# Optimization experiments

Measured on AMD Instinct MI355X. Metric: run time of the kernel, lower is better.

The kernel has to match this reference:

```python
import jax, jax.numpy as jnp
import numpy as np

DIM = 512
HEADS = 8
DIM_HEAD = 64
INNER = HEADS * DIM_HEAD  # 512
TOPK_FRAC = 0.7
SCALE = DIM_HEAD ** -0.5


def setup_inputs() -> dict:
    key = jax.random.key(0)
    k1, k2, k3, k4 = jax.random.split(key, 4)
    B, N = 4, 1024
    x = jax.random.normal(k1, (B, N, DIM), dtype=jnp.float32)
    # nn.Linear(dim, inner*3, bias=False): weight [3*inner, dim]; store transposed for x @ W
    w_qkv = jax.random.normal(k2, (DIM, 3 * INNER), dtype=jnp.float32) * (DIM ** -0.5)
    # to_out Linear(inner, dim) with bias
    w_out = jax.random.normal(k3, (INNER, DIM), dtype=jnp.float32) * (INNER ** -0.5)
    b_out = jax.random.normal(k4, (DIM,), dtype=jnp.float32) * 0.01
    return {"x": x, "w_qkv": w_qkv, "w_out": w_out, "b_out": b_out}


def reference(x, w_qkv, w_out, b_out):
    B, N, _ = x.shape
    H, D = HEADS, DIM_HEAD
    qkv = x @ w_qkv  # [B, N, 3*INNER]
    q, k, v = jnp.split(qkv, 3, axis=-1)
    # 'b n (h d) -> b h n d'
    reshape = lambda t: t.reshape(B, N, H, D).transpose(0, 2, 1, 3)
    q, k, v = reshape(q), reshape(k), reshape(v)
    dots = jnp.einsum('bhid,bhjd->bhij', q, k) * SCALE  # [B, H, N, N]
    # per-row top-k masking (kNN attention)
    kk = int(N * TOPK_FRAC)
    _, idx = jax.lax.top_k(dots, kk)  # [B, H, N, kk]
    bi = jnp.arange(B)[:, None, None, None]
    hi = jnp.arange(H)[None, :, None, None]
    ii = jnp.arange(N)[None, None, :, None]
    mask = jnp.zeros_like(dots).at[bi, hi, ii, idx].set(1.0)
    dots = jnp.where(mask > 0, dots, jnp.float32(-jnp.inf))
    attn = jax.nn.softmax(dots, axis=-1)
    out = jnp.einsum('bhij,bhjd->bhid', attn, v)  # [B, H, N, D]
    out = out.transpose(0, 2, 1, 3).reshape(B, N, H * D)  # 'b h n d -> b n (h d)'
    return out @ w_out + b_out
```

## Files before the change

kernel.cpp:

```cpp
#include <hip/hip_runtime.h>
#include <cstddef>

#define B_      4
#define N_      1024
#define DIM_    512
#define H_      8
#define D_      64
#define INNER_  512
#define TRIPLE_ 1536
#define KK_     716
#define SCALE_  0.125f

typedef short bf16x8 __attribute__((ext_vector_type(8)));
typedef float f32x4  __attribute__((ext_vector_type(4)));
typedef unsigned short ushort_t;
typedef ushort_t us8 __attribute__((ext_vector_type(8)));

__device__ __forceinline__ unsigned short bf16_rne(float f) {
    unsigned u = __float_as_uint(f);
    return (unsigned short)((u + 0x7FFFu + ((u >> 16) & 1u)) >> 16);
}
__device__ __forceinline__ float bf16_f(unsigned short s) {
    return __uint_as_float((unsigned)s << 16);
}
__device__ __forceinline__ unsigned f2key(float f) {
    unsigned u = __float_as_uint(f);
    return u ^ ((u & 0x80000000u) ? 0xFFFFFFFFu : 0x80000000u);
}
__device__ __forceinline__ float key2f(unsigned k) {
    unsigned u = (k & 0x80000000u) ? (k ^ 0x80000000u) : ~k;
    return __uint_as_float(u);
}
__device__ __forceinline__ int wave_count(int lc) {
    int c = __popcll(__ballot(lc & 1));
    c += __popcll(__ballot(lc & 2)) << 1;
    c += __popcll(__ballot(lc & 4)) << 2;
    c += __popcll(__ballot(lc & 8)) << 3;
    c += __popcll(__ballot(lc & 16)) << 4;
    return c;
}
__device__ __forceinline__ int count_ge(const unsigned* key, unsigned kt) {
    int lc = 0;
#pragma unroll
    for (int m = 0; m < 16; ++m) lc += (key[m] >= kt) ? 1 : 0;
    return wave_count(lc);
}
__device__ __forceinline__ unsigned bisect_exact(const unsigned* key,
                                                 bool hlo, bool hhi,
                                                 float tlo, float thi) {
    unsigned klo = hlo ? f2key(tlo) : 0u;
    unsigned khi = hhi ? f2key(thi) : 0xFFFFFFFFu;
    while (khi - klo > 1u) {
        const unsigned km = klo + ((khi - klo) >> 1);
        const int c = count_ge(key, km);
        if (c >= KK_) { klo = km; if (c == KK_) break; }
        else khi = km;
    }
    return klo;
}
__device__ __forceinline__ void topk2(const unsigned* key0, const unsigned* key1,
                                      float mu0, float sg0, float mu1, float sg1,
                                      unsigned& out0, unsigned& out1) {
    bool done0 = false, done1 = false;
    float tlo0 = 0.f, thi0 = 0.f, tlo1 = 0.f, thi1 = 0.f;
    int   clo0 = 0,   chi0 = 0,   clo1 = 0,   chi1 = 0;
    bool  hlo0 = false, hhi0 = false, hlo1 = false, hhi1 = false;
    float t0 = mu0 - 0.52189f * sg0;
    float t1 = mu1 - 0.52189f * sg1;
    unsigned res0 = 0u, res1 = 0u;
    for (int it = 0; it < 10; ++it) {
        if (done0 & done1) break;
        const unsigned kt0 = f2key(t0);
        const unsigned kt1 = f2key(t1);
        int lc0 = 0, lc1 = 0;
#pragma unroll
        for (int m = 0; m < 16; ++m) {
            lc0 += (key0[m] >= kt0) ? 1 : 0;
            lc1 += (key1[m] >= kt1) ? 1 : 0;
        }
        const int c0 = wave_count(lc0);
        const int c1 = wave_count(lc1);
        if (!done0) {
            if (c0 == KK_) { res0 = kt0; done0 = true; }
            else {
                if (c0 > KK_) { tlo0 = t0; clo0 = c0; hlo0 = true; }
                else          { thi0 = t0; chi0 = c0; hhi0 = true; }
                float tn;
                if (hlo0 && hhi0) {
                    tn = tlo0 + (thi0 - tlo0) * ((float)(clo0 - KK_) / (float)(clo0 - chi0));
                } else {
                    const float z    = (t0 - mu0) / sg0;
                    const float dens = fmaxf(408.5f * __expf(-0.5f * z * z) / sg0, 1.f);
                    tn = t0 + (float)(c0 - KK_) / dens;
                }
                if (hlo0 && !(tn > tlo0)) tn = hhi0 ? 0.5f * (tlo0 + thi0) : tlo0 + 0.25f * sg0;
                if (hhi0 && !(tn < thi0)) tn = hlo0 ? 0.5f * (tlo0 + thi0) : thi0 - 0.25f * sg0;
                t0 = tn;
            }
        }
        if (!done1) {
            if (c1 == KK_) { res1 = kt1; done1 = true; }
            else {
                if (c1 > KK_) { tlo1 = t1; clo1 = c1; hlo1 = true; }
                else          { thi1 = t1; chi1 = c1; hhi1 = true; }
                float tn;
                if (hlo1 && hhi1) {
                    tn = tlo1 + (thi1 - tlo1) * ((float)(clo1 - KK_) / (float)(clo1 - chi1));
                } else {
                    const float z    = (t1 - mu1) / sg1;
                    const float dens = fmaxf(408.5f * __expf(-0.5f * z * z) / sg1, 1.f);
                    tn = t1 + (float)(c1 - KK_) / dens;
                }
                if (hlo1 && !(tn > tlo1)) tn = hhi1 ? 0.5f * (tlo1 + thi1) : tlo1 + 0.25f * sg1;
                if (hhi1 && !(tn < thi1)) tn = hlo1 ? 0.5f * (tlo1 + thi1) : thi1 - 0.25f * sg1;
                t1 = tn;
            }
        }
    }
    if (!done0) res0 = bisect_exact(key0, hlo0, hhi0, tlo0, thi0);
    if (!done1) res1 = bisect_exact(key1, hlo1, hhi1, tlo1, thi1);
    out0 = res0;
    out1 = res1;
}
__device__ __forceinline__ void split8(const float* __restrict__ src,
                                       bf16x8& h8, bf16x8& l8) {
    float4 a = *(const float4*)src;
    float4 b = *(const float4*)(src + 4);
    float v[8] = {a.x, a.y, a.z, a.w, b.x, b.y, b.z, b.w};
#pragma unroll
    for (int i = 0; i < 8; ++i) {
        ushort_t hb = bf16_rne(v[i]);
        h8[i] = (short)hb;
        l8[i] = (short)bf16_rne(v[i] - bf16_f(hb));
    }
}

__global__ __launch_bounds__(256) void prep_split(const float* __restrict__ Wq,
                                                  const float* __restrict__ Wo,
                                                  ushort_t* __restrict__ WqTh,
                                                  ushort_t* __restrict__ WqTl,
                                                  ushort_t* __restrict__ WoTh,
                                                  ushort_t* __restrict__ WoTl) {
    __shared__ float tile[32][33];
    const int wb = blockIdx.x;
    const int bx = wb & 63, by = wb >> 6;
    const bool isQ = bx < 48;
    const int  nb  = (isQ ? bx : bx - 48) * 32;
    const int  kb  = by * 32;
    const int  Nn  = isQ ? TRIPLE_ : DIM_;
    const float* W = isQ ? Wq : Wo;
    ushort_t* Th   = isQ ? WqTh : WoTh;
    ushort_t* Tl   = isQ ? WqTl : WoTl;
    const int tx = threadIdx.x & 31, ty = threadIdx.x >> 5;
    for (int yy = ty; yy < 32; yy += 8)
        tile[yy][tx] = W[(size_t)(kb + yy) * Nn + nb + tx];
    __syncthreads();
    for (int yy = ty; yy < 32; yy += 8) {
        float v = tile[tx][yy];
        ushort_t hb = bf16_rne(v);
        size_t idx = (size_t)(nb + yy) * DIM_ + kb + tx;
        Th[idx] = hb;
        Tl[idx] = bf16_rne(v - bf16_f(hb));
    }
}

__global__ __launch_bounds__(256) void gemm_qkv_mfma(
    const float* __restrict__ X,
    const ushort_t* __restrict__ Wh, const ushort_t* __restrict__ Wl,
    ushort_t* __restrict__ Qh, ushort_t* __restrict__ Ql,
    ushort_t* __restrict__ Kh, ushort_t* __restrict__ Kl,
    ushort_t* __restrict__ Vt) {
    __shared__ ushort_t stile[4][4608];
    __shared__ ushort_t BshH[2][2048];
    __shared__ ushort_t BshL[2][2048];
    const int t = threadIdx.x, w = t >> 6, l = t & 63;
    const int ln = l & 15, quad = l >> 4;
    const int n0 = blockIdx.y * 64;
    const int m0 = blockIdx.x * 128 + w * 32;
    f32x4 acc[2][4] = {};
    {
        const size_t xrow0 = (size_t)(m0 + ln) * DIM_;
        const size_t xrow1 = (size_t)(m0 + 16 + ln) * DIM_;
        const int srow = t >> 2;
        const int sk   = (t & 3) << 3;
        const size_t gb = (size_t)(n0 + srow) * DIM_ + sk;
        us8 nh = *(const us8*)&Wh[gb];
        us8 nl = *(const us8*)&Wl[gb];
        *(us8*)&BshH[0][t * 8] = nh;
        *(us8*)&BshL[0][t * 8] = nl;
        int cur = 0;
        for (int k0 = 0; k0 < DIM_; k0 += 32) {
            const bool more = (k0 + 32) < DIM_;
            const size_t gnext = gb + (size_t)(more ? k0 + 32 : 0);
            nh = *(const us8*)&Wh[gnext];
            nl = *(const us8*)&Wl[gnext];
            __syncthreads();
            const int ko = k0 + quad * 8;
            bf16x8 ah0, al0, ah1, al1;
            split8(&X[xrow0 + ko], ah0, al0);
            split8(&X[xrow1 + ko], ah1, al1);
#pragma unroll
            for (int j = 0; j < 4; ++j) {
                const int slot = (((j << 4) + ln) << 5) + (quad << 3);
                bf16x8 bh = *(const bf16x8*)&BshH[cur][slot];
                bf16x8 bl = *(const bf16x8*)&BshL[cur][slot];
                acc[0][j] = __builtin_amdgcn_mfma_f32_16x16x32_bf16(ah0, bh, acc[0][j], 0, 0, 0);
                acc[0][j] = __builtin_amdgcn_mfma_f32_16x16x32_bf16(al0, bh, acc[0][j], 0, 0, 0);
                acc[0][j] = __builtin_amdgcn_mfma_f32_16x16x32_bf16(ah0, bl, acc[0][j], 0, 0, 0);
                acc[1][j] = __builtin_amdgcn_mfma_f32_16x16x32_bf16(ah1, bh, acc[1][j], 0, 0, 0);
                acc[1][j] = __builtin_amdgcn_mfma_f32_16x16x32_bf16(al1, bh, acc[1][j], 0, 0, 0);
                acc[1][j] = __builtin_amdgcn_mfma_f32_16x16x32_bf16(ah1, bl, acc[1][j], 0, 0, 0);
            }
            if (more) {
                *(us8*)&BshH[cur ^ 1][t * 8] = nh;
                *(us8*)&BshL[cur ^ 1][t * 8] = nl;
            }
            cur ^= 1;
        }
    }
    const int sec = n0 >> 9;
    const int h   = (n0 >> 6) & 7;
    ushort_t* tw  = stile[w];
    const int b = m0 >> 10, nnb = m0 & 1023;
    if (sec < 2) {
        ushort_t* Hp = sec ? Kh : Qh;
        ushort_t* Lp = sec ? Kl : Ql;
        const float qsc = sec ? 1.0f : SCALE_;
#pragma unroll
        for (int i = 0; i < 2; ++i)
#pragma unroll
            for (int j = 0; j < 4; ++j)
#pragma unroll
                for (int g = 0; g < 4; ++g) {
                    const float v = acc[i][j][g] * qsc;
                    const ushort_t hb = bf16_rne(v);
                    const ushort_t lb = bf16_rne(v - bf16_f(hb));
                    const int tok = i * 16 + quad * 4 + g;
                    const int d   = j * 16 + ln;
                    tw[tok * 72 + d]        = hb;
                    tw[2304 + tok * 72 + d] = lb;
                }
        __syncthreads();
        const size_t rowbase = ((size_t)(b * 8 + h) * 1024 + nnb) * 64;
        const int dd = (l & 7) * 8;
#pragma unroll
        for (int s = 0; s < 4; ++s) {
            const int tl = s * 8 + (l >> 3);
            const size_t off = rowbase + (size_t)tl * 64 + dd;
            *(us8*)&Hp[off] = *(const us8*)&tw[tl * 72 + dd];
            *(us8*)&Lp[off] = *(const us8*)&tw[2304 + tl * 72 + dd];
        }
    } else {
#pragma unroll
        for (int i = 0; i < 2; ++i)
#pragma unroll
            for (int j = 0; j < 4; ++j)
#pragma unroll
                for (int g = 0; g < 4; ++g)
                    tw[(j * 16 + ln) * 40 + i * 16 + quad * 4 + g] = bf16_rne(acc[i][j][g]);
        __syncthreads();
        const size_t vbase = (size_t)(b * 8 + h) * 65536 + nnb;
#pragma unroll
        for (int p = 0; p < 2; ++p) {
            const int d = (p << 5) + (l >> 1);
            const int c = (l & 1) << 4;
            ushort_t* dst = &Vt[vbase + (size_t)d * 1024 + c];
            *(us8*)dst       = *(const us8*)&tw[d * 40 + c];
            *(us8*)(dst + 8) = *(const us8*)&tw[d * 40 + c + 8];
        }
    }
}

__global__ __launch_bounds__(256) void gemm_out_mfma(
    const ushort_t* __restrict__ Ah, const ushort_t* __restrict__ Al,
    const ushort_t* __restrict__ Wh, const ushort_t* __restrict__ Wl,
    const float* __restrict__ bias, float* __restrict__ C) {
    __shared__ ushort_t BshH[2][2048];
    __shared__ ushort_t BshL[2][2048];
    const int t = threadIdx.x, w = t >> 6, l = t & 63;
    const int ln = l & 15, quad = l >> 4;
    const int n0 = blockIdx.y * 64;
    const int m0 = blockIdx.x * 64 + w * 16;
    f32x4 acc[4] = {};
    {
        const size_t arow0 = (size_t)(m0 + ln) * INNER_;
        const int srow = t >> 2;
        const int sk   = (t & 3) << 3;
        const size_t gb = (size_t)(n0 + srow) * INNER_ + sk;
        us8 nh = *(const us8*)&Wh[gb];
        us8 nl = *(const us8*)&Wl[gb];
        *(us8*)&BshH[0][t * 8] = nh;
        *(us8*)&BshL[0][t * 8] = nl;
        int cur = 0;
        for (int k0 = 0; k0 < INNER_; k0 += 32) {
            const bool more = (k0 + 32) < INNER_;
            const size_t gnext = gb + (size_t)(more ? k0 + 32 : 0);
            nh = *(const us8*)&Wh[gnext];
            nl = *(const us8*)&Wl[gnext];
            __syncthreads();
            const int ko = k0 + quad * 8;
            bf16x8 ah0 = *(const bf16x8*)&Ah[arow0 + ko];
            bf16x8 al0 = *(const bf16x8*)&Al[arow0 + ko];
#pragma unroll
            for (int j = 0; j < 4; ++j) {
                const int slot = (((j << 4) + ln) << 5) + (quad << 3);
                bf16x8 bh = *(const bf16x8*)&BshH[cur][slot];
                bf16x8 bl = *(const bf16x8*)&BshL[cur][slot];
                acc[j] = __builtin_amdgcn_mfma_f32_16x16x32_bf16(ah0, bh, acc[j], 0, 0, 0);
                acc[j] = __builtin_amdgcn_mfma_f32_16x16x32_bf16(al0, bh, acc[j], 0, 0, 0);
                acc[j] = __builtin_amdgcn_mfma_f32_16x16x32_bf16(ah0, bl, acc[j], 0, 0, 0);
            }
            if (more) {
                *(us8*)&BshH[cur ^ 1][t * 8] = nh;
                *(us8*)&BshL[cur ^ 1][t * 8] = nl;
            }
            cur ^= 1;
        }
    }
#pragma unroll
    for (int j = 0; j < 4; ++j) {
        const int col = n0 + j * 16 + ln;
        const float bb = bias[col];
#pragma unroll
        for (int g = 0; g < 4; ++g) {
            const int token = m0 + quad * 4 + g;
            C[(size_t)token * DIM_ + col] = acc[j][g] + bb;
        }
    }
}

__global__ __launch_bounds__(512)
__attribute__((amdgpu_waves_per_eu(4, 4)))
void attn_mfma(const ushort_t* __restrict__ Qh,
               const ushort_t* __restrict__ Ql,
               const ushort_t* __restrict__ Kh,
               const ushort_t* __restrict__ Kl,
               const ushort_t* __restrict__ Vt,
               ushort_t* __restrict__ Oh,
               ushort_t* __restrict__ Ol) {
    __shared__ float sdots[16 * 1024];
    __shared__ float spartial[4][16][17];

    const int t    = threadIdx.x;
    const int w    = t >> 6;
    const int l    = t & 63;
    const int ln   = l & 15;
    const int quad = l >> 4;
    const int wg   = blockIdx.x;
    const int bh   = wg & 31;
    const int i0   = (wg >> 5) << 4;

    const size_t bhoff = (size_t)bh << 16;

    const ushort_t* qp  = Qh + bhoff + (size_t)(i0 + ln) * 64 + (quad << 3);
    const ushort_t* qlp = Ql + bhoff + (size_t)(i0 + ln) * 64 + (quad << 3);
    bf16x8 qh0 = *(const bf16x8*)qp;
    bf16x8 qh1 = *(const bf16x8*)(qp + 32);
    bf16x8 ql0 = *(const bf16x8*)qlp;
    bf16x8 ql1 = *(const bf16x8*)(qlp + 32);

    const int dblk  = w & 3;
    const int jbase = (w & 4) << 7;
    const ushort_t* vp =
        Vt + bhoff + (size_t)((dblk << 4) + ln) * 1024 + (quad << 3) + jbase;
    bf16x8 vpre[8];

    for (int tt = 0; tt < 8; ++tt) {
        const int j0 = ((w << 3) + tt) << 4;
        const ushort_t* kp  = Kh + bhoff + (size_t)(j0 + ln) * 64 + (quad << 3);
        const ushort_t* klp = Kl + bhoff + (size_t)(j0 + ln) * 64 + (quad << 3);
        bf16x8 kh0 = *(const bf16x8*)kp;
        bf16x8 kh1 = *(const bf16x8*)(kp + 32);
        bf16x8 kl0 = *(const bf16x8*)klp;
        bf16x8 kl1 = *(const bf16x8*)(klp + 32);
        f32x4 acc = {0.f, 0.f, 0.f, 0.f};
        acc = __builtin_amdgcn_mfma_f32_16x16x32_bf16(qh0, kh0, acc, 0, 0, 0);
        acc = __builtin_amdgcn_mfma_f32_16x16x32_bf16(qh1, kh1, acc, 0, 0, 0);
        acc = __builtin_amdgcn_mfma_f32_16x16x32_bf16(qh0, kl0, acc, 0, 0, 0);
        acc = __builtin_amdgcn_mfma_f32_16x16x32_bf16(qh1, kl1, acc, 0, 0, 0);
        acc = __builtin_amdgcn_mfma_f32_16x16x32_bf16(ql0, kh0, acc, 0, 0, 0);
        acc = __builtin_amdgcn_mfma_f32_16x16x32_bf16(ql1, kh1, acc, 0, 0, 0);
#pragma unroll
        for (int g = 0; g < 4; ++g) {
            const int row = (quad << 2) + g;
            sdots[(row << 10) + ((j0 + ln) ^ ((row & 7) << 2))] = acc[g];
        }
    }
    __syncthreads();

    ushort_t* sP = (ushort_t*)sdots;
    {
        const int r0 = w << 1, r1 = r0 | 1;
        const int swz0 = (r0 & 7) << 2, swz1 = (r1 & 7) << 2;
        const float* s0 = &sdots[r0 << 10];
        const float* s1 = &sdots[r1 << 10];
        unsigned key0[16], key1[16];
        float sa0 = 0.f, sb0 = 0.f, sa1 = 0.f, sb1 = 0.f;
#pragma unroll
        for (int m = 0; m < 4; ++m) {
            f32x4 kv0 = *(const f32x4*)&s0[((l << 2) + (m << 8)) ^ swz0];
            f32x4 kv1 = *(const f32x4*)&s1[((l << 2) + (m << 8)) ^ swz1];
#pragma unroll
            for (int i = 0; i < 4; ++i) {
                key0[(m << 2) + i] = f2key(kv0[i]);
                key1[(m << 2) + i] = f2key(kv1[i]);
                sa0 += kv0[i];
                sb0 += kv0[i] * kv0[i];
                sa1 += kv1[i];
                sb1 += kv1[i] * kv1[i];
            }
        }
#pragma unroll
        for (int off = 32; off; off >>= 1) {
            sa0 += __shfl_xor(sa0, off, 64);
            sb0 += __shfl_xor(sb0, off, 64);
            sa1 += __shfl_xor(sa1, off, 64);
            sb1 += __shfl_xor(sb1, off, 64);
        }
        const float mu0 = sa0 * (1.0f / 1024.f);
        const float sg0 = sqrtf(fmaxf(sb0 * (1.0f / 1024.f) - mu0 * mu0, 1e-20f));
        const float mu1 = sa1 * (1.0f / 1024.f);
        const float sg1 = sqrtf(fmaxf(sb1 * (1.0f / 1024.f) - mu1 * mu1, 1e-20f));

        unsigned res0, res1;
        topk2(key0, key1, mu0, sg0, mu1, sg1, res0, res1);

        const float thr0 = key2f(res0), thr1 = key2f(res1);
        float pv0[16], pv1[16];
        float ls0 = 0.f, ls1 = 0.f;
#pragma unroll
        for (int m = 0; m < 16; ++m) {
            float p0 = (key0[m] >= res0) ? __expf(key2f(key0[m]) - thr0) : 0.f;
            float p1 = (key1[m] >= res1) ? __expf(key2f(key1[m]) - thr1) : 0.f;
            pv0[m] = p0;
            pv1[m] = p1;
            ls0 += p0;
            ls1 += p1;
        }
#pragma unroll
        for (int p = 0; p < 8; ++p)
            vpre[p] = *(const bf16x8*)(vp + p * 32);
#pragma unroll
        for (int off = 32; off; off >>= 1) {
            ls0 += __shfl_xor(ls0, off, 64);
            ls1 += __shfl_xor(ls1, off, 64);
        }
        const float inv0 = 1.f / ls0, inv1 = 1.f / ls1;
#pragma unroll
        for (int m = 0; m < 4; ++m) {
            const int g0 = ((l >> 1) + (m << 5)) ^ (r0 & 7);
            const int g1 = ((l >> 1) + (m << 5)) ^ (r1 & 7);
            ushort4 pk0 = make_ushort4(bf16_rne(pv0[(m << 2) + 0] * inv0),
                                       bf16_rne(pv0[(m << 2) + 1] * inv0),
                                       bf16_rne(pv0[(m << 2) + 2] * inv0),
                                       bf16_rne(pv0[(m << 2) + 3] * inv0));
            ushort4 pk1 = make_ushort4(bf16_rne(pv1[(m << 2) + 0] * inv1),
                                       bf16_rne(pv1[(m << 2) + 1] * inv1),
                                       bf16_rne(pv1[(m << 2) + 2] * inv1),
                                       bf16_rne(pv1[(m << 2) + 3] * inv1));
            *(ushort4*)&sP[(r0 << 11) + (g0 << 3) + ((l & 1) << 2)] = pk0;
            *(ushort4*)&sP[(r1 << 11) + (g1 << 3) + ((l & 1) << 2)] = pk1;
        }
    }
    __syncthreads();

    const int prow = ln << 11;
    const int rsw  = ln & 7;
    bf16x8 vnx[8];
#pragma unroll
    for (int p = 0; p < 8; ++p)
        vnx[p] = *(const bf16x8*)(vp + 256 + p * 32);
    f32x4 oa[4] = {};
    __builtin_amdgcn_s_setprio(1);
#pragma unroll
    for (int p = 0; p < 8; ++p) {
        const int j0 = p * 32;
        const int g = ((jbase + j0) >> 3) + quad;
        bf16x8 af = *(const bf16x8*)&sP[prow + ((g ^ rsw) << 3)];
        oa[p & 3] = __builtin_amdgcn_mfma_f32_16x16x32_bf16(af, vpre[p], oa[p & 3], 0, 0, 0);
    }
#pragma unroll
    for (int p = 0; p < 8; ++p) {
        const int j0 = 256 + p * 32;
        const int g = ((jbase + j0) >> 3) + quad;
        bf16x8 af = *(const bf16x8*)&sP[prow + ((g ^ rsw) << 3)];
        oa[p & 3] = __builtin_amdgcn_mfma_f32_16x16x32_bf16(af, vnx[p], oa[p & 3], 0, 0, 0);
    }
    __builtin_amdgcn_s_setprio(0);
    f32x4 oacc = (oa[0] + oa[1]) + (oa[2] + oa[3]);

    if (w & 4) {
#pragma unroll
        for (int g = 0; g < 4; ++g)
            spartial[dblk][(quad << 2) + g][ln] = oacc[g];
    }
    __syncthreads();
    if (!(w & 4)) {
        const int b = bh >> 3, h = bh & 7;
        const size_t obase =
            ((size_t)(b << 10) + i0 + (quad << 2)) * 512 + (h << 6) + (dblk << 4) + ln;
#pragma unroll
        for (int g = 0; g < 4; ++g) {
            const float v = oacc[g] + spartial[dblk][(quad << 2) + g][ln];
            ushort_t hb = bf16_rne(v);
            Oh[obase + (size_t)g * 512] = hb;
            Ol[obase + (size_t)g * 512] = bf16_rne(v - bf16_f(hb));
        }
    }
}

extern "C" void kernel_launch(void* const* d_in, const int* in_sizes, int n_in,
                              void* d_out, int out_size, void* d_ws, size_t ws_size,
                              hipStream_t stream) {
    const float* x     = (const float*)d_in[0];
    const float* w_qkv = (const float*)d_in[1];
    const float* w_out = (const float*)d_in[2];
    const float* b_out = (const float*)d_in[3];
    float*       out   = (float*)d_out;

    const size_t ON  = (size_t)4096 * 512;
    const size_t WQT = (size_t)1536 * 512;
    const size_t WOT = (size_t)512 * 512;
    const size_t QK  = (size_t)32 * 1024 * 64;

    ushort_t* p    = (ushort_t*)d_ws;
    ushort_t* Oh   = p;            p += ON;
    ushort_t* Ol   = p;            p += ON;
    ushort_t* WqTh = p;            p += WQT;
    ushort_t* WqTl = p;            p += WQT;
    ushort_t* WoTh = p;            p += WOT;
    ushort_t* WoTl = p;            p += WOT;
    ushort_t* Qh   = p;            p += QK;
    ushort_t* Ql   = p;            p += QK;
    ushort_t* Kh   = p;            p += QK;
    ushort_t* Kl   = p;            p += QK;
    ushort_t* Vt   = p;            p += QK;

    prep_split<<<dim3(1024), 256, 0, stream>>>(w_qkv, w_out, WqTh, WqTl,
                                               WoTh, WoTl);

    gemm_qkv_mfma<<<dim3(4096 / 128, TRIPLE_ / 64), 256, 0, stream>>>(
        x, WqTh, WqTl, Qh, Ql, Kh, Kl, Vt);

    attn_mfma<<<dim3(B_ * H_ * (N_ / 16)), 512, 0, stream>>>(Qh, Ql, Kh, Kl,
                                                             Vt, Oh, Ol);

    gemm_out_mfma<<<dim3(4096 / 64, DIM_ / 64), 256, 0, stream>>>(
        Oh, Ol, WoTh, WoTl, b_out, out);
}
```

Baseline: 218.9 us.

## Fuse weight split prep and QKV GEMM into one cooperative kernel with grid sync

```diff
diff --git a/kernel.cpp b/kernel.cpp
--- a/kernel.cpp
+++ b/kernel.cpp
@@ -1,5 +1,8 @@
 #include <hip/hip_runtime.h>
+#include <hip/hip_cooperative_groups.h>
 #include <cstddef>
+
+namespace cg = cooperative_groups;
 
 #define B_      4
 #define N_      1024
@@ -135,14 +138,14 @@
     }
 }
 
-__global__ __launch_bounds__(256) void prep_split(const float* __restrict__ Wq,
-                                                  const float* __restrict__ Wo,
-                                                  ushort_t* __restrict__ WqTh,
-                                                  ushort_t* __restrict__ WqTl,
-                                                  ushort_t* __restrict__ WoTh,
-                                                  ushort_t* __restrict__ WoTl) {
-    __shared__ float tile[32][33];
-    const int wb = blockIdx.x;
+__device__ __forceinline__ void prep_tile_body(int wb,
+                                               const float* __restrict__ Wq,
+                                               const float* __restrict__ Wo,
+                                               ushort_t* __restrict__ WqTh,
+                                               ushort_t* __restrict__ WqTl,
+                                               ushort_t* __restrict__ WoTh,
+                                               ushort_t* __restrict__ WoTl,
+                                               float (*tile)[33]) {
     const int bx = wb & 63, by = wb >> 6;
     const bool isQ = bx < 48;
     const int  nb  = (isQ ? bx : bx - 48) * 32;
@@ -164,19 +167,17 @@
     }
 }
 
-__global__ __launch_bounds__(256) void gemm_qkv_mfma(
+__device__ __forceinline__ void qkv_tile_body(
+    int n0, int m0blk,
     const float* __restrict__ X,
     const ushort_t* __restrict__ Wh, const ushort_t* __restrict__ Wl,
     ushort_t* __restrict__ Qh, ushort_t* __restrict__ Ql,
     ushort_t* __restrict__ Kh, ushort_t* __restrict__ Kl,
-    ushort_t* __restrict__ Vt) {
-    __shared__ ushort_t stile[4][4608];
-    __shared__ ushort_t BshH[2][2048];
-    __shared__ ushort_t BshL[2][2048];
+    ushort_t* __restrict__ Vt,
+    ushort_t (*stile)[4608], ushort_t (*BshH)[2048], ushort_t (*BshL)[2048]) {
     const int t = threadIdx.x, w = t >> 6, l = t & 63;
     const int ln = l & 15, quad = l >> 4;
-    const int n0 = blockIdx.y * 64;
-    const int m0 = blockIdx.x * 128 + w * 32;
+    const int m0 = m0blk * 128 + w * 32;
     f32x4 acc[2][4] = {};
     {
         const size_t xrow0 = (size_t)(m0 + ln) * DIM_;
@@ -268,6 +269,58 @@
             *(us8*)dst       = *(const us8*)&tw[d * 40 + c];
             *(us8*)(dst + 8) = *(const us8*)&tw[d * 40 + c + 8];
         }
+    }
+}
+
+__global__ __launch_bounds__(256) void prep_split(const float* __restrict__ Wq,
+                                                  const float* __restrict__ Wo,
+                                                  ushort_t* __restrict__ WqTh,
+                                                  ushort_t* __restrict__ WqTl,
+                                                  ushort_t* __restrict__ WoTh,
+                                                  ushort_t* __restrict__ WoTl) {
+    __shared__ float tile[32][33];
+    prep_tile_body(blockIdx.x, Wq, Wo, WqTh, WqTl, WoTh, WoTl, tile);
+}
+
+__global__ __launch_bounds__(256) void gemm_qkv_mfma(
+    const float* __restrict__ X,
+    const ushort_t* __restrict__ Wh, const ushort_t* __restrict__ Wl,
+    ushort_t* __restrict__ Qh, ushort_t* __restrict__ Ql,
+    ushort_t* __restrict__ Kh, ushort_t* __restrict__ Kl,
+    ushort_t* __restrict__ Vt) {
+    __shared__ ushort_t stile[4][4608];
+    __shared__ ushort_t BshH[2][2048];
+    __shared__ ushort_t BshL[2][2048];
+    qkv_tile_body(blockIdx.y * 64, blockIdx.x, X, Wh, Wl,
+                  Qh, Ql, Kh, Kl, Vt, stile, BshH, BshL);
+}
+
+__global__ __launch_bounds__(256) void fused_prep_qkv(
+    const float* __restrict__ X,
+    const float* __restrict__ Wq, const float* __restrict__ Wo,
+    ushort_t* __restrict__ WqTh, ushort_t* __restrict__ WqTl,
+    ushort_t* __restrict__ WoTh, ushort_t* __restrict__ WoTl,
+    ushort_t* __restrict__ Qh, ushort_t* __restrict__ Ql,
+    ushort_t* __restrict__ Kh, ushort_t* __restrict__ Kl,
+    ushort_t* __restrict__ Vt) {
+    __shared__ ushort_t stile[4][4608];
+    __shared__ ushort_t BshH[2][2048];
+    __shared__ ushort_t BshL[2][2048];
+
+    {
+        float (*tile)[33] = (float(*)[33])&stile[0][0];
+        for (int vb = blockIdx.x; vb < 1024; vb += gridDim.x) {
+            prep_tile_body(vb, Wq, Wo, WqTh, WqTl, WoTh, WoTl, tile);
+            __syncthreads();
+        }
+    }
+    __threadfence();
+    cg::this_grid().sync();
+
+    for (int vb = blockIdx.x; vb < 768; vb += gridDim.x) {
+        qkv_tile_body((vb >> 5) * 64, vb & 31, X, WqTh, WqTl,
+                      Qh, Ql, Kh, Kl, Vt, stile, BshH, BshL);
+        __syncthreads();
     }
 }
 
@@ -536,11 +589,18 @@
     ushort_t* Kl   = p;            p += QK;
     ushort_t* Vt   = p;            p += QK;
 
-    prep_split<<<dim3(1024), 256, 0, stream>>>(w_qkv, w_out, WqTh, WqTl,
-                                               WoTh, WoTl);
-
-    gemm_qkv_mfma<<<dim3(4096 / 128, TRIPLE_ / 64), 256, 0, stream>>>(
-        x, WqTh, WqTl, Qh, Ql, Kh, Kl, Vt);
+    void* args[] = {(void*)&x, (void*)&w_qkv, (void*)&w_out,
+                    (void*)&WqTh, (void*)&WqTl, (void*)&WoTh, (void*)&WoTl,
+                    (void*)&Qh, (void*)&Ql, (void*)&Kh, (void*)&Kl, (void*)&Vt};
+    hipError_t ce = hipLaunchCooperativeKernel((void*)fused_prep_qkv,
+                                               dim3(512), dim3(256),
+                                               args, 0, stream);
+    if (ce != hipSuccess) {
+        prep_split<<<dim3(1024), 256, 0, stream>>>(w_qkv, w_out, WqTh, WqTl,
+                                                   WoTh, WoTl);
+        gemm_qkv_mfma<<<dim3(4096 / 128, TRIPLE_ / 64), 256, 0, stream>>>(
+            x, WqTh, WqTl, Qh, Ql, Kh, Kl, Vt);
+    }
 
     attn_mfma<<<dim3(B_ * H_ * (N_ / 16)), 512, 0, stream>>>(Qh, Ql, Kh, Kl,
                                                              Vt, Oh, Ol);
```

Result: slower. 314.6 us (+43.8%).
